# Optimization experiments

Hardware: AMD Instinct MI355X
Metric: run time of the kernel (lower is better)

The kernel has to match this reference:

```python
import jax, jax.numpy as jnp
import numpy as np

BATCH = 2048
INPUT_SIZE = 2048
OUTPUT_SIZE = 2048
N_INPUTS = 6            # fan-in per LUT node
K = 1 << N_INPUTS       # 64 table entries per node


def setup_inputs() -> dict:
    key = jax.random.key(0)
    k1, k2, k3 = jax.random.split(key, 3)
    x = jax.random.uniform(k1, (BATCH, INPUT_SIZE), dtype=jnp.float32)
    table = jax.random.normal(k2, (OUTPUT_SIZE, K), dtype=jnp.float32)
    mapping = jax.random.randint(k3, (OUTPUT_SIZE, N_INPUTS), 0, INPUT_SIZE, dtype=jnp.int64)
    return {"x": x, "table": table, "mapping": mapping}


def reference(x, table, mapping):
    # x: (B, I) in [0,1]; table: (O, 2^n) raw logits; mapping: (O, n) int indices
    O, n = mapping.shape
    Kv = 1 << n
    # per-node input gather -> (B, O, n)
    xg = x[:, mapping]
    # binary codes of the 2^n LUT vertices: bits[k, i] = i-th bit of k
    bits = ((jnp.arange(Kv)[:, None] >> jnp.arange(n)[None, :]) & 1).astype(x.dtype)  # (K, n)
    # vertex probabilities prod_i (x_i if bit else 1-x_i), built by a tiny fixed loop over n
    probs = jnp.ones((x.shape[0], O, Kv), dtype=x.dtype)
    for i in range(n):
        xi = xg[:, :, i][:, :, None]                      # (B, O, 1)
        bi = bits[:, i][None, None, :]                    # (1, 1, K)
        probs = probs * (xi * bi + (1.0 - xi) * (1.0 - bi))
    # differentiable LUT lookup: expected table value under vertex distribution
    out = jnp.einsum('bok,ok->bo', probs, jax.nn.sigmoid(table))  # (B, O)
    return out
```

## Files before the change

### kernel.cpp

```cpp
#include <hip/hip_runtime.h>
#include <math.h>

#define B_TOTAL 2048
#define I_TOTAL 2048
#define O_TOTAL 2048
#define KW 64
#define NIN 6
#define BLOCK 256
#define TILE_B 16
#define OBLOCKS (O_TOTAL / BLOCK)
#define BBLOCKS (B_TOTAL / TILE_B)

__global__ void prep_kernel(const float* __restrict__ table,
                            const unsigned int* __restrict__ map_raw,
                            float* __restrict__ sigw,
                            int* __restrict__ m32)
{
    int idx = blockIdx.x * blockDim.x + threadIdx.x;
    const int total = O_TOTAL * KW;
    if (idx < total) {
        float v = table[idx];
        sigw[idx] = 1.0f / (1.0f + __expf(-v));
    }
    const int nmap = O_TOTAL * NIN;
    if (idx < nmap) {
        bool is64 = ((map_raw[1] | map_raw[3] | map_raw[5] | map_raw[7]) == 0u);
        int val = is64 ? (int)map_raw[2 * idx] : (int)map_raw[idx];
        m32[idx] = val;
    }
}

__global__ __launch_bounds__(BLOCK) void lut_main(
    const float* __restrict__ x,
    const float* __restrict__ sigw,
    const int*   __restrict__ m32,
    float*       __restrict__ out)
{
    const int o  = blockIdx.y * BLOCK + threadIdx.x;
    const int b0 = blockIdx.x * TILE_B;

    float ww[KW];
    const float4* wp = (const float4*)(sigw + (size_t)o * KW);
    #pragma unroll
    for (int i = 0; i < KW / 4; ++i) {
        float4 v = wp[i];
        ww[4*i+0] = v.x; ww[4*i+1] = v.y; ww[4*i+2] = v.z; ww[4*i+3] = v.w;
    }

    int m[NIN];
    #pragma unroll
    for (int i = 0; i < NIN; ++i) m[i] = m32[o * NIN + i];

    for (int ib = 0; ib < TILE_B; ++ib) {
        const float* xr = x + (size_t)(b0 + ib) * I_TOTAL;
        float xv[NIN];
        #pragma unroll
        for (int i = 0; i < NIN; ++i) xv[i] = xr[m[i]];

        float t[32];
        #pragma unroll
        for (int j = 0; j < 32; ++j) t[j] = fmaf(xv[5], ww[j+32] - ww[j], ww[j]);
        #pragma unroll
        for (int j = 0; j < 16; ++j) t[j] = fmaf(xv[4], t[j+16] - t[j], t[j]);
        #pragma unroll
        for (int j = 0; j < 8;  ++j) t[j] = fmaf(xv[3], t[j+8]  - t[j], t[j]);
        #pragma unroll
        for (int j = 0; j < 4;  ++j) t[j] = fmaf(xv[2], t[j+4]  - t[j], t[j]);
        #pragma unroll
        for (int j = 0; j < 2;  ++j) t[j] = fmaf(xv[1], t[j+2]  - t[j], t[j]);
        float res = fmaf(xv[0], t[1] - t[0], t[0]);

        out[(size_t)(b0 + ib) * O_TOTAL + o] = res;
    }
}

extern "C" void kernel_launch(void* const* d_in, const int* in_sizes, int n_in,
                              void* d_out, int out_size, void* d_ws, size_t ws_size,
                              hipStream_t stream)
{
    const float*        x       = (const float*)d_in[0];
    const float*        table   = (const float*)d_in[1];
    const unsigned int* map_raw = (const unsigned int*)d_in[2];
    float* out  = (float*)d_out;
    float* sigw = (float*)d_ws;
    int*   m32  = (int*)((char*)d_ws + (size_t)O_TOTAL * KW * sizeof(float));

    prep_kernel<<<(O_TOTAL * KW) / BLOCK, BLOCK, 0, stream>>>(table, map_raw, sigw, m32);

    dim3 grid(BBLOCKS, OBLOCKS);
    lut_main<<<grid, dim3(BLOCK), 0, stream>>>(x, sigw, m32, out);
}
```

Measured before the change: 101.9 us.

## Stage x rows in LDS, transpose weights and mapping, precompute first-level differences

```diff
diff --git a/kernel.cpp b/kernel.cpp
--- a/kernel.cpp
+++ b/kernel.cpp
@@ -8,69 +8,86 @@
 #define NIN 6
 #define BLOCK 256
 #define TILE_B 16
+#define CH 4
+#define BBLOCKS (B_TOTAL / TILE_B)
 #define OBLOCKS (O_TOTAL / BLOCK)
-#define BBLOCKS (B_TOTAL / TILE_B)
 
 __global__ void prep_kernel(const float* __restrict__ table,
                             const unsigned int* __restrict__ map_raw,
-                            float* __restrict__ sigw,
-                            int* __restrict__ m32)
+                            float* __restrict__ wT,
+                            int* __restrict__ m32T)
 {
     int idx = blockIdx.x * blockDim.x + threadIdx.x;
-    const int total = O_TOTAL * KW;
-    if (idx < total) {
-        float v = table[idx];
-        sigw[idx] = 1.0f / (1.0f + __expf(-v));
+    int o = idx >> 6, k = idx & 63;
+    float s = 1.0f / (1.0f + __expf(-table[idx]));
+    float v;
+    if (k >= 32) {
+        float s0 = 1.0f / (1.0f + __expf(-table[idx - 32]));
+        v = s - s0;
+    } else {
+        v = s;
     }
-    const int nmap = O_TOTAL * NIN;
-    if (idx < nmap) {
+    wT[k * O_TOTAL + o] = v;
+
+    if (idx < O_TOTAL * NIN) {
         bool is64 = ((map_raw[1] | map_raw[3] | map_raw[5] | map_raw[7]) == 0u);
         int val = is64 ? (int)map_raw[2 * idx] : (int)map_raw[idx];
-        m32[idx] = val;
+        int oo = idx / NIN, ii = idx - oo * NIN;
+        m32T[ii * O_TOTAL + oo] = val;
     }
 }
 
 __global__ __launch_bounds__(BLOCK) void lut_main(
     const float* __restrict__ x,
-    const float* __restrict__ sigw,
-    const int*   __restrict__ m32,
+    const float* __restrict__ wT,
+    const int*   __restrict__ m32T,
     float*       __restrict__ out)
 {
+    __shared__ float xs[CH * I_TOTAL];
+
     const int o  = blockIdx.y * BLOCK + threadIdx.x;
     const int b0 = blockIdx.x * TILE_B;
 
     float ww[KW];
-    const float4* wp = (const float4*)(sigw + (size_t)o * KW);
     #pragma unroll
-    for (int i = 0; i < KW / 4; ++i) {
-        float4 v = wp[i];
-        ww[4*i+0] = v.x; ww[4*i+1] = v.y; ww[4*i+2] = v.z; ww[4*i+3] = v.w;
-    }
+    for (int k = 0; k < KW; ++k) ww[k] = wT[k * O_TOTAL + o];
 
     int m[NIN];
     #pragma unroll
-    for (int i = 0; i < NIN; ++i) m[i] = m32[o * NIN + i];
+    for (int i = 0; i < NIN; ++i) m[i] = m32T[i * O_TOTAL + o];
 
-    for (int ib = 0; ib < TILE_B; ++ib) {
-        const float* xr = x + (size_t)(b0 + ib) * I_TOTAL;
-        float xv[NIN];
+    #pragma unroll
+    for (int c = 0; c < TILE_B / CH; ++c) {
+        __syncthreads();
+        const float4* src = (const float4*)(x + (size_t)(b0 + c * CH) * I_TOTAL);
+        float4* dst = (float4*)xs;
         #pragma unroll
-        for (int i = 0; i < NIN; ++i) xv[i] = xr[m[i]];
+        for (int t = 0; t < (CH * I_TOTAL / 4) / BLOCK; ++t)
+            dst[t * BLOCK + threadIdx.x] = src[t * BLOCK + threadIdx.x];
+        __syncthreads();
 
-        float t[32];
         #pragma unroll
-        for (int j = 0; j < 32; ++j) t[j] = fmaf(xv[5], ww[j+32] - ww[j], ww[j]);
-        #pragma unroll
-        for (int j = 0; j < 16; ++j) t[j] = fmaf(xv[4], t[j+16] - t[j], t[j]);
-        #pragma unroll
-        for (int j = 0; j < 8;  ++j) t[j] = fmaf(xv[3], t[j+8]  - t[j], t[j]);
-        #pragma unroll
-        for (int j = 0; j < 4;  ++j) t[j] = fmaf(xv[2], t[j+4]  - t[j], t[j]);
-        #pragma unroll
-        for (int j = 0; j < 2;  ++j) t[j] = fmaf(xv[1], t[j+2]  - t[j], t[j]);
-        float res = fmaf(xv[0], t[1] - t[0], t[0]);
+        for (int cr = 0; cr < CH; ++cr) {
+            const float* xr = xs + cr * I_TOTAL;
+            float xv[NIN];
+            #pragma unroll
+            for (int i = 0; i < NIN; ++i) xv[i] = xr[m[i]];
 
-        out[(size_t)(b0 + ib) * O_TOTAL + o] = res;
+            float t[32];
+            #pragma unroll
+            for (int j = 0; j < 32; ++j) t[j] = fmaf(xv[5], ww[j + 32], ww[j]);
+            #pragma unroll
+            for (int j = 0; j < 16; ++j) t[j] = fmaf(xv[4], t[j + 16] - t[j], t[j]);
+            #pragma unroll
+            for (int j = 0; j < 8;  ++j) t[j] = fmaf(xv[3], t[j + 8]  - t[j], t[j]);
+            #pragma unroll
+            for (int j = 0; j < 4;  ++j) t[j] = fmaf(xv[2], t[j + 4]  - t[j], t[j]);
+            #pragma unroll
+            for (int j = 0; j < 2;  ++j) t[j] = fmaf(xv[1], t[j + 2]  - t[j], t[j]);
+            float res = fmaf(xv[0], t[1] - t[0], t[0]);
+
+            out[(size_t)(b0 + c * CH + cr) * O_TOTAL + o] = res;
+        }
     }
 }
 
@@ -82,11 +99,11 @@
     const float*        table   = (const float*)d_in[1];
     const unsigned int* map_raw = (const unsigned int*)d_in[2];
     float* out  = (float*)d_out;
-    float* sigw = (float*)d_ws;
-    int*   m32  = (int*)((char*)d_ws + (size_t)O_TOTAL * KW * sizeof(float));
+    float* wT   = (float*)d_ws;
+    int*   m32T = (int*)((char*)d_ws + (size_t)O_TOTAL * KW * sizeof(float));
 
-    prep_kernel<<<(O_TOTAL * KW) / BLOCK, BLOCK, 0, stream>>>(table, map_raw, sigw, m32);
+    prep_kernel<<<(O_TOTAL * KW) / BLOCK, BLOCK, 0, stream>>>(table, map_raw, wT, m32T);
 
     dim3 grid(BBLOCKS, OBLOCKS);
-    lut_main<<<grid, dim3(BLOCK), 0, stream>>>(x, sigw, m32, out);
+    lut_main<<<grid, dim3(BLOCK), 0, stream>>>(x, wT, m32T, out);
 }
```

Result: faster. 84.29 us (-17.3%).
